# Kernel tuning notes

Hardware: AMD Instinct MI355X
Metric: run time of the kernel (lower is better)

## Reference

```python
import jax, jax.numpy as jnp
import numpy as np

B, S, H, I, E_ROUTED, TOP_K = 8, 2048, 1024, 2048, 8, 2


def _expert(x, Wg, Wu, Wd):
    # SwiGLU expert: down(silu(gate(x)) * up(x)); Linear weights stored [out, in]
    return (jax.nn.silu(x @ Wg.T) * (x @ Wu.T)) @ Wd.T


def setup_inputs() -> dict:
    key = jax.random.key(0)
    ks = jax.random.split(key, 9)
    s = 0.02  # init scale
    return {
        "x": jax.random.normal(ks[0], (B, S, H), dtype=jnp.float32),
        # shared expert (num_shared = 1)
        "Wg_s": jax.random.normal(ks[1], (I, H), dtype=jnp.float32) * s,
        "Wu_s": jax.random.normal(ks[2], (I, H), dtype=jnp.float32) * s,
        "Wd_s": jax.random.normal(ks[3], (H, I), dtype=jnp.float32) * s,
        # routed experts, stacked [E, ...]
        "Wg": jax.random.normal(ks[4], (E_ROUTED, I, H), dtype=jnp.float32) * s,
        "Wu": jax.random.normal(ks[5], (E_ROUTED, I, H), dtype=jnp.float32) * s,
        "Wd": jax.random.normal(ks[6], (E_ROUTED, H, I), dtype=jnp.float32) * s,
        # router
        "Wr": jax.random.normal(ks[7], (E_ROUTED, H), dtype=jnp.float32) * s,
        "rb": jnp.zeros((E_ROUTED,), dtype=jnp.float32),
    }


def reference(x, Wg_s, Wu_s, Wd_s, Wg, Wu, Wd, Wr, rb):
    # shared experts (num_shared = 1, so mean == the single expert output)
    shared = _expert(x, Wg_s, Wu_s, Wd_s)  # [B,S,H]

    # sigmoid top-k routing
    logits = jnp.einsum('bsh,eh->bse', x, Wr) + rb        # [B,S,E]
    probs = jax.nn.sigmoid(logits)
    scores, idx = jax.lax.top_k(probs, TOP_K)             # [B,S,K]

    # dense combine weights: cw[b,s,e] = sum_k scores[b,s,k] * 1[idx[b,s,k]==e]
    cw = (jax.nn.one_hot(idx, E_ROUTED, dtype=x.dtype) * scores[..., None]).sum(-2)  # [B,S,E]

    out = shared
    for e in range(E_ROUTED):  # small fixed expert count
        out = out + cw[..., e:e + 1] * _expert(x, Wg[e], Wu[e], Wd[e])
    return out
```

## Files before the change

### kernel.cpp

```cpp
#include <hip/hip_runtime.h>

#define T_TOK 16384
#define HDIM  1024
#define IDIM  2048
#define NEXP  8
#define CNT_STRIDE 32
#define TOK_PER_BLK 32
#define MAX_RTILES 144

typedef __attribute__((ext_vector_type(8))) short bf16x8;
typedef __attribute__((ext_vector_type(4))) float f32x4;
typedef unsigned short u16;
typedef unsigned int u32;

typedef __attribute__((address_space(1))) const unsigned int gas_u32;
typedef __attribute__((address_space(3))) unsigned int las_u32;

__device__ __forceinline__ void gl16(const void* g, void* l) {
  __builtin_amdgcn_global_load_lds((gas_u32*)g, (las_u32*)l, 16, 0, 0);
}

__device__ __forceinline__ u16 f2bf(float f) {
  union { float f; u32 i; } v; v.f = f;
  u32 r = v.i + 0x7FFF + ((v.i >> 16) & 1);
  return (u16)(r >> 16);
}
__device__ __forceinline__ u32 pack2(float a, float b) {
  return (u32)f2bf(a) | ((u32)f2bf(b) << 16);
}

__global__ __launch_bounds__(256) void cvt_kernel(
    const float* __restrict__ s, u16* __restrict__ d, int n)
{
  int i = (blockIdx.x * 256 + threadIdx.x) * 4;
  if (i < n) {
    f32x4 v = *(const f32x4*)(s + i);
    uint2 o; o.x = pack2(v[0], v[1]); o.y = pack2(v[2], v[3]);
    *(uint2*)(d + i) = o;
  }
}

__global__ __launch_bounds__(256) void cvt_gu_kernel(
    const float* __restrict__ Wg, const float* __restrict__ Wu,
    u16* __restrict__ d, int nrows)
{
  int i = (blockIdx.x * 256 + threadIdx.x) * 4;
  if (i >= nrows * 1024) return;
  int r = i >> 10, c = i & 1023;
  int eb = r >> 12;
  int rr = r & 4095;
  int sub = rr & 31, b = rr >> 5;
  const float* s = (sub < 16 ? Wg : Wu) +
                   (((size_t)(eb * IDIM + b * 16 + (sub & 15))) << 10) + c;
  f32x4 v = *(const f32x4*)s;
  uint2 o; o.x = pack2(v[0], v[1]); o.y = pack2(v[2], v[3]);
  *(uint2*)(d + i) = o;
}

__global__ void init_counts(int* counts) {
  counts[threadIdx.x] = 0;
}

__global__ __launch_bounds__(256) void router_kernel(
    const float* __restrict__ x, const float* __restrict__ Wr,
    const float* __restrict__ rb, float* __restrict__ cw,
    int* __restrict__ counts, int* __restrict__ lists)
{
  __shared__ __align__(16) float sWr[NEXP * HDIM];
  __shared__ int pickE[2 * TOK_PER_BLK];
  __shared__ int pickT[2 * TOK_PER_BLK];

  const int tid = threadIdx.x;
  const int lane = tid & 63;
  const int wv = tid >> 6;

  for (int i = tid; i < NEXP * HDIM / 4; i += 256)
    ((f32x4*)sWr)[i] = ((const f32x4*)Wr)[i];

  float rbl[NEXP];
  #pragma unroll
  for (int e = 0; e < NEXP; ++e) rbl[e] = rb[e];

  __syncthreads();

  const int t_base = blockIdx.x * TOK_PER_BLK + wv * (TOK_PER_BLK / 4);
  for (int j = 0; j < TOK_PER_BLK / 4; ++j) {
    const int t = t_base + j;
    const float* xrow = x + (size_t)t * HDIM;
    f32x4 xv[4];
    #pragma unroll
    for (int c = 0; c < 4; ++c) xv[c] = *(const f32x4*)(xrow + c * 256 + lane * 4);

    double acc[NEXP];
    #pragma unroll
    for (int e = 0; e < NEXP; ++e) {
      const float* wr = sWr + e * HDIM;
      double a = 0.0;
      #pragma unroll
      for (int c = 0; c < 4; ++c) {
        f32x4 w4 = *(const f32x4*)(wr + c * 256 + lane * 4);
        a += (double)xv[c][0] * (double)w4[0];
        a += (double)xv[c][1] * (double)w4[1];
        a += (double)xv[c][2] * (double)w4[2];
        a += (double)xv[c][3] * (double)w4[3];
      }
      acc[e] = a;
    }
    #pragma unroll
    for (int e = 0; e < NEXP; ++e) {
      double a = acc[e];
      a += __shfl_xor(a, 1, 64);
      a += __shfl_xor(a, 2, 64);
      a += __shfl_xor(a, 4, 64);
      acc[e] = a;
    }
    double s0 = (lane & 1) ? acc[1] : acc[0];
    double s1 = (lane & 1) ? acc[3] : acc[2];
    double s2 = (lane & 1) ? acc[5] : acc[4];
    double s3 = (lane & 1) ? acc[7] : acc[6];
    double u0 = (lane & 2) ? s1 : s0;
    double u1 = (lane & 2) ? s3 : s2;
    double v  = (lane & 4) ? u1 : u0;
    v += __shfl_xor(v, 8, 64);
    v += __shfl_xor(v, 16, 64);
    v += __shfl_xor(v, 32, 64);
    double l[NEXP];
    #pragma unroll
    for (int e = 0; e < NEXP; ++e) l[e] = __shfl(v, e, 64) + (double)rbl[e];

    if (lane == 0) {
      int i1 = 0;
      #pragma unroll
      for (int e = 1; e < NEXP; ++e) if (l[e] > l[i1]) i1 = e;
      int i2 = -1;
      #pragma unroll
      for (int e = 0; e < NEXP; ++e) {
        if (e == i1) continue;
        if (i2 < 0 || l[e] > l[i2]) i2 = e;
      }
      float p1 = (float)(1.0 / (1.0 + exp(-l[i1])));
      float p2 = (float)(1.0 / (1.0 + exp(-l[i2])));
      cw[(size_t)t * NEXP + i1] = p1;
      cw[(size_t)t * NEXP + i2] = p2;
      int slot = (wv * (TOK_PER_BLK / 4) + j) * 2;
      pickE[slot] = i1; pickE[slot + 1] = i2;
      pickT[slot] = t;  pickT[slot + 1] = t;
    }
  }
  __syncthreads();

  const int myE = pickE[lane];
  const int myT = pickT[lane];
  #pragma unroll
  for (int ei = 0; ei < 2; ++ei) {
    int e = wv + ei * 4;
    unsigned long long b = __ballot(myE == e);
    int cnt = __popcll(b);
    int base = 0;
    if (lane == 0) base = atomicAdd(&counts[e * CNT_STRIDE], cnt);
    base = __shfl(base, 0, 64);
    if (myE == e)
      lists[(size_t)e * T_TOK + base + __popcll(b & ((1ull << lane) - 1))] = myT;
  }
}

__global__ void build_tiles(const int* __restrict__ counts,
                            int* __restrict__ td_e, int* __restrict__ td_r0,
                            int* __restrict__ ntiles)
{
  if (threadIdx.x == 0) {
    int n = 0;
    for (int e = 0; e < NEXP; ++e) {
      int c = counts[e * CNT_STRIDE];
      for (int r = 0; r < c; r += 256) { td_e[n] = e; td_r0[n] = r; ++n; }
    }
    *ntiles = n;
  }
}


template<bool FUSED>
__global__ __launch_bounds__(512, 2) void gateup256(
    const u16* __restrict__ xb, const u16* __restrict__ Wgu,
    const int* __restrict__ lists, const int* __restrict__ counts,
    const int* __restrict__ td_e, const int* __restrict__ td_r0,
    const int* __restrict__ ntiles,
    u16* __restrict__ hbuf, int t0c0)
{
  __shared__ __align__(16) u16 sA[2 * 256 * 64];
  __shared__ __align__(16) u16 sB[2 * 256 * 64];

  int r0, cnt; const int* list = nullptr;
  const u16* W;
  if (FUSED) {
    int ty = t0c0 + blockIdx.y;
    if (ty >= *ntiles) return;
    int e = td_e[ty]; r0 = td_r0[ty]; cnt = counts[e * CNT_STRIDE];
    list = lists + (size_t)e * T_TOK;
    W = Wgu + (size_t)e * 2 * IDIM * HDIM;
  } else {
    r0 = t0c0 + blockIdx.y * 256; cnt = T_TOK;
    W = Wgu;
  }
  const int n0 = blockIdx.x * 256;

  const int tid = threadIdx.x, lane = tid & 63, w = tid >> 6;
  const int wm = w >> 2, wn = w & 3;
  const int quad = lane >> 4, l15 = lane & 15, l7 = lane & 7;

  const int lsub = lane >> 3;
  const int sslot = (lane & 7) ^ lsub;

  const u16 *gA[4], *gB[4];
  u16 *dA[4], *dB[4];
  #pragma unroll
  for (int q = 0; q < 4; ++q) {
    int row = (w * 4 + q) * 8 + lsub;
    int tok;
    if (FUSED) { int gi = r0 + row; tok = (gi < cnt) ? list[gi] : 0; }
    else tok = r0 + row;
    gA[q] = xb + (size_t)tok * HDIM + sslot * 8;
    gB[q] = W + (size_t)(n0 + row) * HDIM + sslot * 8;
    dA[q] = sA + (w * 4 + q) * 512;
    dB[q] = sB + (w * 4 + q) * 512;
  }

  f32x4 acc[8][4] = {};

  const int arow = (wm * 128 + l15) * 64;
  const int brow = (wn * 64 + l15) * 64;
  const int sw0 = ((quad) ^ l7) * 8;
  const int sw1 = ((4 + quad) ^ l7) * 8;

  auto STAGE = [&](int t, int b) {
    int boff = b * 16384;
    #pragma unroll
    for (int q = 0; q < 4; ++q) {
      gl16(gA[q] + t * 64, dA[q] + boff);
      gl16(gB[q] + t * 64, dB[q] + boff);
    }
  };
  auto COMPUTE = [&](int b) {
    int boff = b * 16384;
    #pragma unroll
    for (int ks = 0; ks < 2; ++ks) {
      int sw = ks ? sw1 : sw0;
      bf16x8 bfr[4], afr[8];
      #pragma unroll
      for (int nt = 0; nt < 4; ++nt)
        bfr[nt] = *(const bf16x8*)(sB + boff + brow + nt * 1024 + sw);
      #pragma unroll
      for (int mt = 0; mt < 8; ++mt)
        afr[mt] = *(const bf16x8*)(sA + boff + arow + mt * 1024 + sw);
      __builtin_amdgcn_s_setprio(1);
      #pragma unroll
      for (int nt = 0; nt < 4; ++nt) {
        #pragma unroll
        for (int mt = 0; mt < 8; ++mt)
          acc[mt][nt] = __builtin_amdgcn_mfma_f32_16x16x32_bf16(afr[mt], bfr[nt], acc[mt][nt], 0, 0, 0);
      }
      __builtin_amdgcn_s_setprio(0);
    }
  };

  const int NT = HDIM / 64;
  STAGE(0, 0);
  STAGE(1, 1);
  for (int t = 0; t < NT - 1; ++t) {
    asm volatile("s_waitcnt vmcnt(8)" ::: "memory");
    __builtin_amdgcn_s_barrier();
    __builtin_amdgcn_sched_barrier(0);
    COMPUTE(t & 1);
    asm volatile("" ::: "memory");
    __builtin_amdgcn_s_barrier();
    __builtin_amdgcn_sched_barrier(0);
    if (t + 2 < NT) STAGE(t + 2, t & 1);
  }
  asm volatile("s_waitcnt vmcnt(0)" ::: "memory");
  __builtin_amdgcn_s_barrier();
  __builtin_amdgcn_sched_barrier(0);
  COMPUTE((NT - 1) & 1);

  const size_t hrb = (size_t)blockIdx.y * 256;
  #pragma unroll
  for (int mt = 0; mt < 8; ++mt) {
    #pragma unroll
    for (int i = 0; i < 4; ++i) {
      int rl = wm * 128 + mt * 16 + quad * 4 + i;
      u16* orow = hbuf + (hrb + rl) * IDIM + (n0 >> 1) + wn * 32 + l15;
      #pragma unroll
      for (int j = 0; j < 2; ++j) {
        float g = acc[mt][2 * j][i], u = acc[mt][2 * j + 1][i];
        float h = (g / (1.f + __expf(-g))) * u;
        orow[j * 16] = f2bf(h);
      }
    }
  }
}

template<bool FUSED>
__global__ __launch_bounds__(512, 2) void down256(
    const u16* __restrict__ hbuf, const u16* __restrict__ Wd_b,
    const int* __restrict__ lists, const int* __restrict__ counts,
    const int* __restrict__ td_e, const int* __restrict__ td_r0,
    const int* __restrict__ ntiles,
    const float* __restrict__ cw, float* __restrict__ out, int t0c0)
{
  __shared__ __align__(16) u16 sA[2 * 256 * 64];
  __shared__ __align__(16) u16 sB[2 * 256 * 64];

  int e = 0, r0, cnt; const int* list = nullptr;
  const u16* Wd;
  if (FUSED) {
    int ty = t0c0 + blockIdx.y;
    if (ty >= *ntiles) return;
    e = td_e[ty]; r0 = td_r0[ty]; cnt = counts[e * CNT_STRIDE];
    list = lists + (size_t)e * T_TOK;
    Wd = Wd_b + (size_t)e * IDIM * HDIM;
  } else {
    r0 = t0c0 + blockIdx.y * 256; cnt = T_TOK;
    Wd = Wd_b;
  }
  const int n0 = blockIdx.x * 256;

  const int tid = threadIdx.x, lane = tid & 63, w = tid >> 6;
  const int wm = w >> 2, wn = w & 3;
  const int quad = lane >> 4, l15 = lane & 15, l7 = lane & 7;

  const int lsub = lane >> 3;
  const int sslot = (lane & 7) ^ lsub;

  const u16 *gA[4], *gB[4];
  u16 *dA[4], *dB[4];
  #pragma unroll
  for (int q = 0; q < 4; ++q) {
    int row = (w * 4 + q) * 8 + lsub;
    gA[q] = hbuf + (size_t)(blockIdx.y * 256 + row) * IDIM + sslot * 8;
    gB[q] = Wd + (size_t)(n0 + row) * IDIM + sslot * 8;
    dA[q] = sA + (w * 4 + q) * 512;
    dB[q] = sB + (w * 4 + q) * 512;
  }

  f32x4 acc[8][4] = {};

  const int arow = (wm * 128 + l15) * 64;
  const int brow = (wn * 64 + l15) * 64;
  const int sw0 = ((quad) ^ l7) * 8;
  const int sw1 = ((4 + quad) ^ l7) * 8;

  auto STAGE = [&](int t, int b) {
    int boff = b * 16384;
    #pragma unroll
    for (int q = 0; q < 4; ++q) {
      gl16(gA[q] + t * 64, dA[q] + boff);
      gl16(gB[q] + t * 64, dB[q] + boff);
    }
  };
  auto COMPUTE = [&](int b) {
    int boff = b * 16384;
    #pragma unroll
    for (int ks = 0; ks < 2; ++ks) {
      int sw = ks ? sw1 : sw0;
      bf16x8 bfr[4], afr[8];
      #pragma unroll
      for (int nt = 0; nt < 4; ++nt)
        bfr[nt] = *(const bf16x8*)(sB + boff + brow + nt * 1024 + sw);
      #pragma unroll
      for (int mt = 0; mt < 8; ++mt)
        afr[mt] = *(const bf16x8*)(sA + boff + arow + mt * 1024 + sw);
      __builtin_amdgcn_s_setprio(1);
      #pragma unroll
      for (int nt = 0; nt < 4; ++nt) {
        #pragma unroll
        for (int mt = 0; mt < 8; ++mt)
          acc[mt][nt] = __builtin_amdgcn_mfma_f32_16x16x32_bf16(afr[mt], bfr[nt], acc[mt][nt], 0, 0, 0);
      }
      __builtin_amdgcn_s_setprio(0);
    }
  };

  const int NT = IDIM / 64;
  STAGE(0, 0);
  STAGE(1, 1);
  for (int t = 0; t < NT - 1; ++t) {
    asm volatile("s_waitcnt vmcnt(8)" ::: "memory");
    __builtin_amdgcn_s_barrier();
    __builtin_amdgcn_sched_barrier(0);
    COMPUTE(t & 1);
    asm volatile("" ::: "memory");
    __builtin_amdgcn_s_barrier();
    __builtin_amdgcn_sched_barrier(0);
    if (t + 2 < NT) STAGE(t + 2, t & 1);
  }
  asm volatile("s_waitcnt vmcnt(0)" ::: "memory");
  __builtin_amdgcn_s_barrier();
  __builtin_amdgcn_sched_barrier(0);
  COMPUTE((NT - 1) & 1);

  #pragma unroll
  for (int mt = 0; mt < 8; ++mt) {
    #pragma unroll
    for (int i = 0; i < 4; ++i) {
      int rl = wm * 128 + mt * 16 + quad * 4 + i;
      if (FUSED) {
        if (r0 + rl < cnt) {
          int token = list[r0 + rl];
          float s = cw[(size_t)token * NEXP + e];
          float* orow = out + (size_t)token * HDIM + n0 + wn * 64 + l15;
          #pragma unroll
          for (int nt = 0; nt < 4; ++nt)
            atomicAdd(&orow[nt * 16], s * acc[mt][nt][i]);
        }
      } else {
        int token = r0 + rl;
        float* orow = out + (size_t)token * HDIM + n0 + wn * 64 + l15;
        #pragma unroll
        for (int nt = 0; nt < 4; ++nt)
          orow[nt * 16] = acc[mt][nt][i];
      }
    }
  }
}

template<int SRC>
__global__ __launch_bounds__(256, 2) void moe_gateup_k(
    const u16* __restrict__ xb, const float* __restrict__ xf,
    const u16* __restrict__ Wg_b, const u16* __restrict__ Wu_b,
    const float* __restrict__ Wg_f, const float* __restrict__ Wu_f,
    const int* __restrict__ list, const int* __restrict__ count_ptr,
    u16* __restrict__ hbuf, int c0)
{
  __shared__ __align__(16) u16 sA[128 * 32];
  __shared__ __align__(16) u16 sG[128 * 32];
  __shared__ __align__(16) u16 sU[128 * 32];

  const int cnt = count_ptr ? *count_ptr : T_TOK;
  const int remain = cnt - c0;
  const int m0 = blockIdx.y * 128;
  if (m0 >= remain) return;
  const int n0 = blockIdx.x * 128;

  const int tid = threadIdx.x, lane = tid & 63, w = tid >> 6;
  const int wm = w & 1, wn = w >> 1;
  const int quad = lane >> 4, l15 = lane & 15;

  const int ar = lane >> 3, ac = lane & 7;

  const float *fa[4], *fg[4], *fu[4];
  int frow[4];
  #pragma unroll
  for (int p = 0; p < 4; ++p) {
    int row = w * 32 + p * 8 + ar;
    frow[p] = row;
    int gi = c0 + m0 + row;
    int tok = (gi < cnt) ? (list ? list[gi] : gi) : 0;
    fa[p] = xf + (size_t)tok * HDIM + ac * 4;
    fg[p] = Wg_f + (size_t)(n0 + row) * HDIM + ac * 4;
    fu[p] = Wu_f + (size_t)(n0 + row) * HDIM + ac * 4;
  }

  const u16* fA = sA + (wm * 64 + l15) * 32 + quad * 8;
  const u16* fG = sG + (wn * 64 + l15) * 32 + quad * 8;
  const u16* fU = sU + (wn * 64 + l15) * 32 + quad * 8;

  f32x4 accG[4][4] = {};
  f32x4 accU[4][4] = {};

  for (int kt = 0; kt < HDIM / 32; ++kt) {
    #pragma unroll
    for (int p = 0; p < 4; ++p) {
      f32x4 va = *(const f32x4*)(fa[p] + kt * 32);
      f32x4 vg = *(const f32x4*)(fg[p] + kt * 32);
      f32x4 vu = *(const f32x4*)(fu[p] + kt * 32);
      uint2 oa; oa.x = pack2(va[0], va[1]); oa.y = pack2(va[2], va[3]);
      uint2 og; og.x = pack2(vg[0], vg[1]); og.y = pack2(vg[2], vg[3]);
      uint2 ou; ou.x = pack2(vu[0], vu[1]); ou.y = pack2(vu[2], vu[3]);
      *(uint2*)(sA + frow[p] * 32 + ac * 4) = oa;
      *(uint2*)(sG + frow[p] * 32 + ac * 4) = og;
      *(uint2*)(sU + frow[p] * 32 + ac * 4) = ou;
    }
    __syncthreads();
    bf16x8 a[4];
    #pragma unroll
    for (int mt = 0; mt < 4; ++mt) a[mt] = *(const bf16x8*)(fA + mt * 16 * 32);
    #pragma unroll
    for (int nt = 0; nt < 4; ++nt) {
      bf16x8 bg = *(const bf16x8*)(fG + nt * 16 * 32);
      bf16x8 bu = *(const bf16x8*)(fU + nt * 16 * 32);
      #pragma unroll
      for (int mt = 0; mt < 4; ++mt) {
        accG[mt][nt] = __builtin_amdgcn_mfma_f32_16x16x32_bf16(a[mt], bg, accG[mt][nt], 0, 0, 0);
        accU[mt][nt] = __builtin_amdgcn_mfma_f32_16x16x32_bf16(a[mt], bu, accU[mt][nt], 0, 0, 0);
      }
    }
    __syncthreads();
  }

  #pragma unroll
  for (int mt = 0; mt < 4; ++mt) {
    #pragma unroll
    for (int i = 0; i < 4; ++i) {
      int row = m0 + wm * 64 + mt * 16 + quad * 4 + i;
      if (row < remain) {
        u16* orow = hbuf + (size_t)row * IDIM + n0 + wn * 64 + l15;
        #pragma unroll
        for (int nt = 0; nt < 4; ++nt) {
          float g = accG[mt][nt][i], u = accU[mt][nt][i];
          float h = (g / (1.f + __expf(-g))) * u;
          orow[nt * 16] = f2bf(h);
        }
      }
    }
  }
  (void)xb; (void)Wg_b; (void)Wu_b;
}

template<int SRC>
__global__ __launch_bounds__(256, 2) void moe_down_k(
    const u16* __restrict__ hbuf,
    const u16* __restrict__ Wd_b, const float* __restrict__ Wd_f,
    const int* __restrict__ list, const int* __restrict__ count_ptr,
    const float* __restrict__ cw, int expert, float* __restrict__ out, int c0)
{
  __shared__ __align__(16) u16 sA[128 * 32];
  __shared__ __align__(16) u16 sB[128 * 32];

  const int cnt = count_ptr ? *count_ptr : T_TOK;
  const int remain = cnt - c0;
  const int m0 = blockIdx.y * 128;
  if (m0 >= remain) return;
  const int n0 = blockIdx.x * 128;

  const int tid = threadIdx.x, lane = tid & 63, w = tid >> 6;
  const int wm = w & 1, wn = w >> 1;
  const int quad = lane >> 4, l15 = lane & 15;

  const int srow0 = w * 32 + (lane >> 2);
  const int srow1 = srow0 + 16;
  const int kch = (lane & 3) * 8;
  const int ar = lane >> 3, ac = lane & 7;

  const u16* pa0 = hbuf + (size_t)(m0 + srow0) * IDIM + kch;
  const u16* pa1 = hbuf + (size_t)(m0 + srow1) * IDIM + kch;
  const float* fb[4];
  int frow[4];
  #pragma unroll
  for (int p = 0; p < 4; ++p) {
    int row = w * 32 + p * 8 + ar;
    frow[p] = row;
    fb[p] = Wd_f + (size_t)(n0 + row) * IDIM + ac * 4;
  }

  const u16* fA = sA + (wm * 64 + l15) * 32 + quad * 8;
  const u16* fB = sB + (wn * 64 + l15) * 32 + quad * 8;

  f32x4 acc[4][4] = {};

  for (int kt = 0; kt < IDIM / 32; ++kt) {
    gl16(pa0 + kt * 32, sA + w * 1024);
    gl16(pa1 + kt * 32, sA + w * 1024 + 512);
    #pragma unroll
    for (int p = 0; p < 4; ++p) {
      f32x4 v = *(const f32x4*)(fb[p] + kt * 32);
      uint2 o; o.x = pack2(v[0], v[1]); o.y = pack2(v[2], v[3]);
      *(uint2*)(sB + frow[p] * 32 + ac * 4) = o;
    }
    __syncthreads();
    bf16x8 a[4];
    #pragma unroll
    for (int mt = 0; mt < 4; ++mt) a[mt] = *(const bf16x8*)(fA + mt * 16 * 32);
    #pragma unroll
    for (int nt = 0; nt < 4; ++nt) {
      bf16x8 b = *(const bf16x8*)(fB + nt * 16 * 32);
      #pragma unroll
      for (int mt = 0; mt < 4; ++mt)
        acc[mt][nt] = __builtin_amdgcn_mfma_f32_16x16x32_bf16(a[mt], b, acc[mt][nt], 0, 0, 0);
    }
    __syncthreads();
  }

  #pragma unroll
  for (int mt = 0; mt < 4; ++mt) {
    #pragma unroll
    for (int i = 0; i < 4; ++i) {
      int rl = m0 + wm * 64 + mt * 16 + quad * 4 + i;
      if (rl < remain) {
        int token = list ? list[c0 + rl] : (c0 + rl);
        float s = (expert >= 0) ? cw[(size_t)token * NEXP + expert] : 1.f;
        float* orow = out + (size_t)token * HDIM + n0 + wn * 64 + l15;
        #pragma unroll
        for (int nt = 0; nt < 4; ++nt) {
          float v = s * acc[mt][nt][i];
          if (expert >= 0) v += orow[nt * 16];
          orow[nt * 16] = v;
        }
      }
    }
  }
  (void)Wd_b;
}

extern "C" void kernel_launch(void* const* d_in, const int* in_sizes, int n_in,
                              void* d_out, int out_size, void* d_ws, size_t ws_size,
                              hipStream_t stream) {
  (void)in_sizes; (void)n_in; (void)out_size;
  const float* x    = (const float*)d_in[0];
  const float* Wg_s = (const float*)d_in[1];
  const float* Wu_s = (const float*)d_in[2];
  const float* Wd_s = (const float*)d_in[3];
  const float* Wg   = (const float*)d_in[4];
  const float* Wu   = (const float*)d_in[5];
  const float* Wd   = (const float*)d_in[6];
  const float* Wr   = (const float*)d_in[7];
  const float* rb   = (const float*)d_in[8];
  float* out = (float*)d_out;

  char* ws = (char*)d_ws;
  size_t off = 1024;
  int* counts = (int*)ws;
  int* lists = (int*)(ws + off);  off += (size_t)NEXP * T_TOK * 4;
  float* cw = (float*)(ws + off); off += (size_t)T_TOK * NEXP * 4;
  int* td = (int*)(ws + off);     off += 2304;
  int* td_e = td;
  int* td_r0 = td + MAX_RTILES;
  int* ntiles = td + 2 * MAX_RTILES;

  const size_t WSH = (size_t)IDIM * HDIM;
  const size_t xc_elems = (size_t)T_TOK * HDIM;
  const size_t wc_elems = 3 * WSH + 3 * NEXP * WSH;
  const size_t fast_need = off + (xc_elems + wc_elems) * 2 + (size_t)2048 * IDIM * 2;
  const bool fast = ws_size >= fast_need;

  u16* xc = (u16*)(ws + off);
  u16* wgus_c = xc + (fast ? xc_elems : 0);
  u16* wds_c  = wgus_c + 2 * WSH;
  u16* wgu_c  = wds_c + WSH;
  u16* wd_c   = wgu_c + 16 * WSH;

  size_t hoff = off + (fast ? (xc_elems + wc_elems) * 2 : 0);
  u16* hbuf = (u16*)(ws + hoff);

  size_t avail = (ws_size > hoff) ? (ws_size - hoff) : 0;
  long long capll = (long long)(avail / ((size_t)IDIM * 2));
  int cap = (capll > T_TOK) ? T_TOK : (int)capll;
  cap &= ~255;
  if (cap < 256) cap = 256;
  int nchunks = (T_TOK + cap - 1) / cap;

  init_counts<<<1, NEXP * CNT_STRIDE, 0, stream>>>(counts);
  if (fast) {
    auto cv = [&](const float* s, u16* d, size_t n) {
      int blocks = (int)((n / 4 + 255) / 256);
      cvt_kernel<<<blocks, 256, 0, stream>>>(s, d, (int)n);
    };
    cv(x, xc, xc_elems);
    cv(Wd_s, wds_c, WSH);
    cv(Wd, wd_c, NEXP * WSH);
    {
      int nrows = 2 * IDIM;
      int blocks = (nrows * 1024 / 4 + 255) / 256;
      cvt_gu_kernel<<<blocks, 256, 0, stream>>>(Wg_s, Wu_s, wgus_c, nrows);
      nrows = NEXP * 2 * IDIM;
      blocks = (nrows * 1024 / 4 + 255) / 256;
      cvt_gu_kernel<<<blocks, 256, 0, stream>>>(Wg, Wu, wgu_c, nrows);
    }
  }
  router_kernel<<<T_TOK / TOK_PER_BLK, 256, 0, stream>>>(x, Wr, rb, cw, counts, lists);

  if (fast) {
    for (int c = 0; c < nchunks; ++c) {
      int c0 = c * cap;
      int rows = (T_TOK - c0 < cap) ? (T_TOK - c0) : cap;
      dim3 g1(2 * IDIM / 256, rows / 256), g2(HDIM / 256, rows / 256);
      gateup256<false><<<g1, 512, 0, stream>>>(xc, wgus_c, nullptr, nullptr,
                                               nullptr, nullptr, nullptr, hbuf, c0);
      down256<false><<<g2, 512, 0, stream>>>(hbuf, wds_c, nullptr, nullptr,
                                             nullptr, nullptr, nullptr, nullptr, out, c0);
    }
    build_tiles<<<1, 64, 0, stream>>>(counts, td_e, td_r0, ntiles);
    int tpc = cap / 256;
    for (int t0 = 0; t0 < MAX_RTILES; t0 += tpc) {
      int yt = (MAX_RTILES - t0 < tpc) ? (MAX_RTILES - t0) : tpc;
      gateup256<true><<<dim3(2 * IDIM / 256, yt), 512, 0, stream>>>(
          xc, wgu_c, lists, counts, td_e, td_r0, ntiles, hbuf, t0);
      down256<true><<<dim3(HDIM / 256, yt), 512, 0, stream>>>(
          hbuf, wd_c, lists, counts, td_e, td_r0, ntiles, cw, out, t0);
    }
  } else {
    dim3 blk(256);
    dim3 gA(IDIM / 128, cap / 128);
    dim3 gB(HDIM / 128, cap / 128);
    for (int c = 0; c < nchunks; ++c) {
      int c0 = c * cap;
      moe_gateup_k<1><<<gA, blk, 0, stream>>>(nullptr, x, nullptr, nullptr, Wg_s, Wu_s,
                                              nullptr, nullptr, hbuf, c0);
      moe_down_k<1><<<gB, blk, 0, stream>>>(hbuf, nullptr, Wd_s, nullptr, nullptr,
                                            cw, -1, out, c0);
    }
    for (int e = 0; e < NEXP; ++e) {
      const int* lst = lists + (size_t)e * T_TOK;
      const int* cptr = counts + (size_t)e * CNT_STRIDE;
      for (int c = 0; c < nchunks; ++c) {
        int c0 = c * cap;
        moe_gateup_k<1><<<gA, blk, 0, stream>>>(nullptr, x, nullptr, nullptr,
                                                Wg + (size_t)e * WSH, Wu + (size_t)e * WSH,
                                                lst, cptr, hbuf, c0);
        moe_down_k<1><<<gB, blk, 0, stream>>>(hbuf, nullptr, Wd + (size_t)e * WSH,
                                              lst, cptr, cw, e, out, c0);
      }
    }
  }
}
```

Before: 1.297 ms.

## Restructure 256x256 GEMM main loops into 4-phase interleaved load/MFMA pipeline

Rewrites the main loop of the gate-up and down GEMM kernels. Each 64-wide K tile is split into two 32-wide halves stored in separate LDS regions with a new XOR swizzle. Every half is computed as L/H quarter passes over the M rows, with the global-to-LDS loads for the next tile issued between the MFMA phases. The aim is finer-grained overlap of memory traffic, LDS reads and matrix math, and lower register pressure from holding fewer A fragments at once. In exchange it adds more barriers per tile, and the tight waitcnt accounting could stall or be wrong if miscounted.

Result: slower. 1.419 ms (+9.4%).

```diff
diff --git a/kernel.cpp b/kernel.cpp
--- a/kernel.cpp
+++ b/kernel.cpp
@@ -179,6 +179,31 @@
 }
 
 
+__device__ __forceinline__ void ld_a4(const u16* baseA, int arow, bf16x8 (&af)[4]) {
+  #pragma unroll
+  for (int i = 0; i < 4; ++i) af[i] = *(const bf16x8*)(baseA + arow + i * 512);
+}
+__device__ __forceinline__ void ld_b4(const u16* baseB, int brow, bf16x8 (&bf)[4]) {
+  #pragma unroll
+  for (int n = 0; n < 4; ++n) bf[n] = *(const bf16x8*)(baseB + brow + n * 512);
+}
+__device__ __forceinline__ void mfma16q(bf16x8 (&af)[4], bf16x8 (&bf)[4],
+                                        f32x4 (&aq)[4][4]) {
+  __builtin_amdgcn_s_setprio(1);
+  #pragma unroll
+  for (int n = 0; n < 4; ++n) {
+    #pragma unroll
+    for (int i = 0; i < 4; ++i)
+      aq[i][n] = __builtin_amdgcn_mfma_f32_16x16x32_bf16(af[i], bf[n], aq[i][n], 0, 0, 0);
+  }
+  __builtin_amdgcn_s_setprio(0);
+}
+#define PH_OPEN()  do { __builtin_amdgcn_s_barrier(); \
+    asm volatile("s_waitcnt lgkmcnt(0)" ::: "memory"); \
+    __builtin_amdgcn_sched_barrier(0); } while (0)
+#define PH_CLOSE() __builtin_amdgcn_s_barrier()
+#define VMW(n) asm volatile("s_waitcnt vmcnt(" #n ")" ::: "memory")
+
 template<bool FUSED>
 __global__ __launch_bounds__(512, 2) void gateup256(
     const u16* __restrict__ xb, const u16* __restrict__ Wgu,
@@ -187,8 +212,8 @@
     const int* __restrict__ ntiles,
     u16* __restrict__ hbuf, int t0c0)
 {
-  __shared__ __align__(16) u16 sA[2 * 256 * 64];
-  __shared__ __align__(16) u16 sB[2 * 256 * 64];
+  __shared__ __align__(16) u16 sA[2 * 2 * 256 * 32];
+  __shared__ __align__(16) u16 sB[2 * 2 * 256 * 32];
 
   int r0, cnt; const int* list = nullptr;
   const u16* W;
@@ -206,80 +231,69 @@
 
   const int tid = threadIdx.x, lane = tid & 63, w = tid >> 6;
   const int wm = w >> 2, wn = w & 3;
-  const int quad = lane >> 4, l15 = lane & 15, l7 = lane & 7;
-
-  const int lsub = lane >> 3;
-  const int sslot = (lane & 7) ^ lsub;
-
-  const u16 *gA[4], *gB[4];
-  u16 *dA[4], *dB[4];
-  #pragma unroll
-  for (int q = 0; q < 4; ++q) {
-    int row = (w * 4 + q) * 8 + lsub;
+  const int quad = lane >> 4, l15 = lane & 15;
+
+  const int srow = (lane >> 2);
+  const int q = (lane & 3) ^ ((lane >> 3) & 3);
+
+  const u16 *pA[2], *pB[2];
+  u16 *dA[2], *dB[2];
+  #pragma unroll
+  for (int i = 0; i < 2; ++i) {
+    int row = w * 32 + i * 16 + srow;
     int tok;
     if (FUSED) { int gi = r0 + row; tok = (gi < cnt) ? list[gi] : 0; }
     else tok = r0 + row;
-    gA[q] = xb + (size_t)tok * HDIM + sslot * 8;
-    gB[q] = W + (size_t)(n0 + row) * HDIM + sslot * 8;
-    dA[q] = sA + (w * 4 + q) * 512;
-    dB[q] = sB + (w * 4 + q) * 512;
-  }
-
-  f32x4 acc[8][4] = {};
-
-  const int arow = (wm * 128 + l15) * 64;
-  const int brow = (wn * 64 + l15) * 64;
-  const int sw0 = ((quad) ^ l7) * 8;
-  const int sw1 = ((4 + quad) ^ l7) * 8;
-
-  auto STAGE = [&](int t, int b) {
-    int boff = b * 16384;
-    #pragma unroll
-    for (int q = 0; q < 4; ++q) {
-      gl16(gA[q] + t * 64, dA[q] + boff);
-      gl16(gB[q] + t * 64, dB[q] + boff);
-    }
+    pA[i] = xb + (size_t)tok * HDIM + q * 8;
+    pB[i] = W + (size_t)(n0 + row) * HDIM + q * 8;
+    dA[i] = sA + (w * 32 + i * 16) * 32;
+    dB[i] = sB + (w * 32 + i * 16) * 32;
+  }
+
+  const int swz = (quad ^ ((l15 >> 1) & 3)) * 8;
+  const int arow = (wm * 128 + l15) * 32 + swz;
+  const int brow = (wn * 64 + l15) * 32 + swz;
+
+  f32x4 accL[4][4] = {};
+  f32x4 accH[4][4] = {};
+
+  auto STAGE_A = [&](int t, int b, int h) {
+    #pragma unroll
+    for (int i = 0; i < 2; ++i)
+      gl16(pA[i] + (size_t)t * 64 + h * 32, dA[i] + b * 16384 + h * 8192);
   };
-  auto COMPUTE = [&](int b) {
-    int boff = b * 16384;
-    #pragma unroll
-    for (int ks = 0; ks < 2; ++ks) {
-      int sw = ks ? sw1 : sw0;
-      bf16x8 bfr[4], afr[8];
-      #pragma unroll
-      for (int nt = 0; nt < 4; ++nt)
-        bfr[nt] = *(const bf16x8*)(sB + boff + brow + nt * 1024 + sw);
-      #pragma unroll
-      for (int mt = 0; mt < 8; ++mt)
-        afr[mt] = *(const bf16x8*)(sA + boff + arow + mt * 1024 + sw);
-      __builtin_amdgcn_s_setprio(1);
-      #pragma unroll
-      for (int nt = 0; nt < 4; ++nt) {
-        #pragma unroll
-        for (int mt = 0; mt < 8; ++mt)
-          acc[mt][nt] = __builtin_amdgcn_mfma_f32_16x16x32_bf16(afr[mt], bfr[nt], acc[mt][nt], 0, 0, 0);
-      }
-      __builtin_amdgcn_s_setprio(0);
-    }
+  auto STAGE_B = [&](int t, int b, int h) {
+    #pragma unroll
+    for (int i = 0; i < 2; ++i)
+      gl16(pB[i] + (size_t)t * 64 + h * 32, dB[i] + b * 16384 + h * 8192);
   };
 
   const int NT = HDIM / 64;
-  STAGE(0, 0);
-  STAGE(1, 1);
-  for (int t = 0; t < NT - 1; ++t) {
-    asm volatile("s_waitcnt vmcnt(8)" ::: "memory");
-    __builtin_amdgcn_s_barrier();
-    __builtin_amdgcn_sched_barrier(0);
-    COMPUTE(t & 1);
-    asm volatile("" ::: "memory");
-    __builtin_amdgcn_s_barrier();
-    __builtin_amdgcn_sched_barrier(0);
-    if (t + 2 < NT) STAGE(t + 2, t & 1);
-  }
-  asm volatile("s_waitcnt vmcnt(0)" ::: "memory");
+  STAGE_A(0, 0, 0); STAGE_B(0, 0, 0);
+  STAGE_A(0, 0, 1); STAGE_B(0, 0, 1);
+  VMW(4);
   __builtin_amdgcn_s_barrier();
-  __builtin_amdgcn_sched_barrier(0);
-  COMPUTE((NT - 1) & 1);
+
+  for (int t = 0; t < NT; ++t) {
+    const int cur = t & 1, nb = cur ^ 1;
+    const int tn = (t + 1 < NT) ? t + 1 : t;
+    const u16* cA = sA + cur * 16384;
+    const u16* cB = sB + cur * 16384;
+    bf16x8 af[4], bf[4];
+    ld_a4(cA, arow, af); ld_b4(cB, brow, bf);
+    STAGE_A(tn, nb, 0);
+    PH_OPEN(); mfma16q(af, bf, accL); PH_CLOSE();
+    ld_a4(cA + 2048, arow, af);
+    STAGE_B(tn, nb, 0);
+    PH_OPEN(); mfma16q(af, bf, accH); VMW(4); PH_CLOSE();
+    ld_a4(cA + 8192, arow, af); ld_b4(cB + 8192, brow, bf);
+    STAGE_A(tn, nb, 1);
+    PH_OPEN(); mfma16q(af, bf, accL); PH_CLOSE();
+    ld_a4(cA + 8192 + 2048, arow, af);
+    STAGE_B(tn, nb, 1);
+    PH_OPEN(); mfma16q(af, bf, accH); VMW(4); PH_CLOSE();
+  }
+  VMW(0);
 
   const size_t hrb = (size_t)blockIdx.y * 256;
   #pragma unroll
@@ -290,7 +304,8 @@
       u16* orow = hbuf + (hrb + rl) * IDIM + (n0 >> 1) + wn * 32 + l15;
       #pragma unroll
       for (int j = 0; j < 2; ++j) {
-        float g = acc[mt][2 * j][i], u = acc[mt][2 * j + 1][i];
+        float g = (mt < 4) ? accL[mt][2 * j][i]     : accH[mt - 4][2 * j][i];
+        float u = (mt < 4) ? accL[mt][2 * j + 1][i] : accH[mt - 4][2 * j + 1][i];
         float h = (g / (1.f + __expf(-g))) * u;
         orow[j * 16] = f2bf(h);
       }
@@ -306,8 +321,8 @@
     const int* __restrict__ ntiles,
     const float* __restrict__ cw, float* __restrict__ out, int t0c0)
 {
-  __shared__ __align__(16) u16 sA[2 * 256 * 64];
-  __shared__ __align__(16) u16 sB[2 * 256 * 64];
+  __shared__ __align__(16) u16 sA[2 * 2 * 256 * 32];
+  __shared__ __align__(16) u16 sB[2 * 2 * 256 * 32];
 
   int e = 0, r0, cnt; const int* list = nullptr;
   const u16* Wd;
@@ -325,83 +340,73 @@
 
   const int tid = threadIdx.x, lane = tid & 63, w = tid >> 6;
   const int wm = w >> 2, wn = w & 3;
-  const int quad = lane >> 4, l15 = lane & 15, l7 = lane & 7;
-
-  const int lsub = lane >> 3;
-  const int sslot = (lane & 7) ^ lsub;
-
-  const u16 *gA[4], *gB[4];
-  u16 *dA[4], *dB[4];
-  #pragma unroll
-  for (int q = 0; q < 4; ++q) {
-    int row = (w * 4 + q) * 8 + lsub;
-    gA[q] = hbuf + (size_t)(blockIdx.y * 256 + row) * IDIM + sslot * 8;
-    gB[q] = Wd + (size_t)(n0 + row) * IDIM + sslot * 8;
-    dA[q] = sA + (w * 4 + q) * 512;
-    dB[q] = sB + (w * 4 + q) * 512;
-  }
-
-  f32x4 acc[8][4] = {};
-
-  const int arow = (wm * 128 + l15) * 64;
-  const int brow = (wn * 64 + l15) * 64;
-  const int sw0 = ((quad) ^ l7) * 8;
-  const int sw1 = ((4 + quad) ^ l7) * 8;
-
-  auto STAGE = [&](int t, int b) {
-    int boff = b * 16384;
-    #pragma unroll
-    for (int q = 0; q < 4; ++q) {
-      gl16(gA[q] + t * 64, dA[q] + boff);
-      gl16(gB[q] + t * 64, dB[q] + boff);
-    }
+  const int quad = lane >> 4, l15 = lane & 15;
+
+  const int srow = (lane >> 2);
+  const int q = (lane & 3) ^ ((lane >> 3) & 3);
+
+  const u16 *pA[2], *pB[2];
+  u16 *dA[2], *dB[2];
+  #pragma unroll
+  for (int i = 0; i < 2; ++i) {
+    int row = w * 32 + i * 16 + srow;
+    pA[i] = hbuf + (size_t)(blockIdx.y * 256 + row) * IDIM + q * 8;
+    pB[i] = Wd + (size_t)(n0 + row) * IDIM + q * 8;
+    dA[i] = sA + (w * 32 + i * 16) * 32;
+    dB[i] = sB + (w * 32 + i * 16) * 32;
+  }
+
+  const int swz = (quad ^ ((l15 >> 1) & 3)) * 8;
+  const int arow = (wm * 128 + l15) * 32 + swz;
+  const int brow = (wn * 64 + l15) * 32 + swz;
+
+  f32x4 accL[4][4] = {};
+  f32x4 accH[4][4] = {};
+
+  auto STAGE_A = [&](int t, int b, int h) {
+    #pragma unroll
+    for (int i = 0; i < 2; ++i)
+      gl16(pA[i] + (size_t)t * 64 + h * 32, dA[i] + b * 16384 + h * 8192);
   };
-  auto COMPUTE = [&](int b) {
-    int boff = b * 16384;
-    #pragma unroll
-    for (int ks = 0; ks < 2; ++ks) {
-      int sw = ks ? sw1 : sw0;
-      bf16x8 bfr[4], afr[8];
-      #pragma unroll
-      for (int nt = 0; nt < 4; ++nt)
-        bfr[nt] = *(const bf16x8*)(sB + boff + brow + nt * 1024 + sw);
-      #pragma unroll
-      for (int mt = 0; mt < 8; ++mt)
-        afr[mt] = *(const bf16x8*)(sA + boff + arow + mt * 1024 + sw);
-      __builtin_amdgcn_s_setprio(1);
-      #pragma unroll
-      for (int nt = 0; nt < 4; ++nt) {
-        #pragma unroll
-        for (int mt = 0; mt < 8; ++mt)
-          acc[mt][nt] = __builtin_amdgcn_mfma_f32_16x16x32_bf16(afr[mt], bfr[nt], acc[mt][nt], 0, 0, 0);
-      }
-      __builtin_amdgcn_s_setprio(0);
-    }
+  auto STAGE_B = [&](int t, int b, int h) {
+    #pragma unroll
+    for (int i = 0; i < 2; ++i)
+      gl16(pB[i] + (size_t)t * 64 + h * 32, dB[i] + b * 16384 + h * 8192);
   };
 
   const int NT = IDIM / 64;
-  STAGE(0, 0);
-  STAGE(1, 1);
-  for (int t = 0; t < NT - 1; ++t) {
-    asm volatile("s_waitcnt vmcnt(8)" ::: "memory");
-    __builtin_amdgcn_s_barrier();
-    __builtin_amdgcn_sched_barrier(0);
-    COMPUTE(t & 1);
-    asm volatile("" ::: "memory");
-    __builtin_amdgcn_s_barrier();
-    __builtin_amdgcn_sched_barrier(0);
-    if (t + 2 < NT) STAGE(t + 2, t & 1);
-  }
-  asm volatile("s_waitcnt vmcnt(0)" ::: "memory");
+  STAGE_A(0, 0, 0); STAGE_B(0, 0, 0);
+  STAGE_A(0, 0, 1); STAGE_B(0, 0, 1);
+  VMW(4);
   __builtin_amdgcn_s_barrier();
-  __builtin_amdgcn_sched_barrier(0);
-  COMPUTE((NT - 1) & 1);
+
+  for (int t = 0; t < NT; ++t) {
+    const int cur = t & 1, nb = cur ^ 1;
+    const int tn = (t + 1 < NT) ? t + 1 : t;
+    const u16* cA = sA + cur * 16384;
+    const u16* cB = sB + cur * 16384;
+    bf16x8 af[4], bf[4];
+    ld_a4(cA, arow, af); ld_b4(cB, brow, bf);
+    STAGE_A(tn, nb, 0);
+    PH_OPEN(); mfma16q(af, bf, accL); PH_CLOSE();
+    ld_a4(cA + 2048, arow, af);
+    STAGE_B(tn, nb, 0);
+    PH_OPEN(); mfma16q(af, bf, accH); VMW(4); PH_CLOSE();
+    ld_a4(cA + 8192, arow, af); ld_b4(cB + 8192, brow, bf);
+    STAGE_A(tn, nb, 1);
+    PH_OPEN(); mfma16q(af, bf, accL); PH_CLOSE();
+    ld_a4(cA + 8192 + 2048, arow, af);
+    STAGE_B(tn, nb, 1);
+    PH_OPEN(); mfma16q(af, bf, accH); VMW(4); PH_CLOSE();
+  }
+  VMW(0);
 
   #pragma unroll
   for (int mt = 0; mt < 8; ++mt) {
     #pragma unroll
     for (int i = 0; i < 4; ++i) {
       int rl = wm * 128 + mt * 16 + quad * 4 + i;
+      f32x4* accp = (mt < 4) ? &accL[mt][0] : &accH[mt - 4][0];
       if (FUSED) {
         if (r0 + rl < cnt) {
           int token = list[r0 + rl];
@@ -409,14 +414,14 @@
           float* orow = out + (size_t)token * HDIM + n0 + wn * 64 + l15;
           #pragma unroll
           for (int nt = 0; nt < 4; ++nt)
-            atomicAdd(&orow[nt * 16], s * acc[mt][nt][i]);
+            atomicAdd(&orow[nt * 16], s * accp[nt][i]);
         }
       } else {
         int token = r0 + rl;
         float* orow = out + (size_t)token * HDIM + n0 + wn * 64 + l15;
         #pragma unroll
         for (int nt = 0; nt < 4; ++nt)
-          orow[nt * 16] = acc[mt][nt][i];
+          orow[nt * 16] = accp[nt][i];
       }
     }
   }
```
